# Kernel optimization log

Hardware: AMD Instinct MI355X
Metric: run time of the kernel (lower is better)

The kernel has to match this reference:

```python
import jax, jax.numpy as jnp
import numpy as np

DIM, HEADS, DH = 512, 8, 64  # head_dim = DIM // HEADS, power of 2
BATCH, SEQ = 2, 1024
RANK = 4  # TensorTrain rank
EPS = 1e-8


def setup_inputs() -> dict:
    key = jax.random.key(0)
    ks = jax.random.split(key, 13)
    inp = {"x": jax.random.normal(ks[0], (BATCH, SEQ, DIM), jnp.float32)}
    i = 1
    for n in ("q", "k", "v", "o"):
        inp[n + "A"] = jax.random.normal(ks[i], (DIM, RANK), jnp.float32) * 0.1
        inp[n + "B"] = jax.random.normal(ks[i + 1], (RANK, DIM), jnp.float32) * 0.1
        inp[n + "b"] = jax.random.normal(ks[i + 2], (DIM,), jnp.float32) * 0.02
        i += 3
    return inp


def _tt_linear(x, A, Bm, b):
    # QuantumInspiredLinear: W = A @ Bm (rank-4 TT reconstruction), y = x W^T + b
    w = A @ Bm  # [out, in]
    return jnp.einsum('bsd,od->bso', x, w) + b


def _embed(x):
    # quantum state preparation: L2-normalize amplitudes per state
    return x / (jnp.linalg.norm(x, axis=-1, keepdims=True) + EPS)


def _measure(x):
    # measurement: squared amplitudes normalized to a probability distribution
    sq = x * x
    return sq / (jnp.sum(sq, axis=-1, keepdims=True) + EPS)


def reference(x, qA, qB, qb, kA, kB, kb, vA, vB, vb, oA, oB, ob):
    bsz, seq, dim = x.shape
    q = _tt_linear(x, qA, qB, qb).reshape(-1, DH)  # [N, dh], N = B*S*H
    k = _tt_linear(x, kA, kB, kb).reshape(-1, DH)
    v = _tt_linear(x, vA, vB, vb).reshape(-1, DH)
    qq = _embed(q)
    kq = _embed(k)
    # flat global attention over N = batch*seq*heads rows (as written in source)
    attn = jax.nn.softmax(jnp.matmul(qq, kq.T) / np.float32(np.sqrt(DH)), axis=-1)
    attended = jnp.matmul(attn, v)           # [N, dh]
    attended = _measure(attended)
    out = attended.reshape(bsz, seq, dim)    # [B, S, D]
    return _tt_linear(out, oA, oB, ob)
```

## Files before the change

### kernel.cpp

```cpp
#include <hip/hip_runtime.h>
#include <math.h>

#define DIM    512
#define RANK   4
#define NROW   2048
#define DH     64
#define NH     16384
#define EPS    1e-8f
#define EPSDEN2 2.68435456f
#define KSCALE 0.0626220703125f
#define C1 (2.0f * KSCALE)
#define C2 (2.0f * KSCALE * KSCALE)
#define KSPL 32

typedef short    bf16x8 __attribute__((ext_vector_type(8)));
typedef ushort   u16x8  __attribute__((ext_vector_type(8)));
typedef _Float16 half8  __attribute__((ext_vector_type(8)));
typedef float    f32x16 __attribute__((ext_vector_type(16)));

static __device__ __forceinline__ ushort f2bf(float f) {
    uint u = __float_as_uint(f);
    u += 0x7FFFu + ((u >> 16) & 1u);
    return (ushort)(u >> 16);
}
static __device__ __forceinline__ float bf2f(ushort u) {
    return __uint_as_float((uint)u << 16);
}
static __device__ __forceinline__ uint pkh2(float a, float b) {
    _Float16 ha = (_Float16)a, hb = (_Float16)b;
    return (uint)__builtin_bit_cast(ushort, ha) | ((uint)__builtin_bit_cast(ushort, hb) << 16);
}
static __device__ __forceinline__ float h2f(ushort u) {
    return (float)__builtin_bit_cast(_Float16, u);
}
static __device__ __forceinline__ void barrier_lgkm() {
    asm volatile("s_waitcnt lgkmcnt(0)" ::: "memory");
    __builtin_amdgcn_s_barrier();
}

__global__ __launch_bounds__(256) void proj_qkv(
    const float* __restrict__ x,
    const float* __restrict__ qA, const float* __restrict__ qB, const float* __restrict__ qb,
    const float* __restrict__ kA, const float* __restrict__ kB, const float* __restrict__ kb,
    const float* __restrict__ vA, const float* __restrict__ vB, const float* __restrict__ vb,
    ushort* __restrict__ qq_b, ushort* __restrict__ kqT, ushort* __restrict__ vvT)
{
    __shared__ float qrow[DIM], krow[DIM], vrowS[DIM];
    __shared__ float wred[4][12];
    __shared__ float tvals[12];
    __shared__ float norms[16];

    const int n = blockIdx.x, t = threadIdx.x;
    const int wid = t >> 6, lane = t & 63;

    const float x0 = x[n * DIM + t];
    const float x1 = x[n * DIM + t + 256];

    float p[12];
    #pragma unroll
    for (int r = 0; r < 4; ++r) {
        p[r]     = x0 * qB[r * DIM + t] + x1 * qB[r * DIM + t + 256];
        p[4 + r] = x0 * kB[r * DIM + t] + x1 * kB[r * DIM + t + 256];
        p[8 + r] = x0 * vB[r * DIM + t] + x1 * vB[r * DIM + t + 256];
    }
    #pragma unroll
    for (int i = 0; i < 12; ++i) {
        #pragma unroll
        for (int off = 32; off; off >>= 1) p[i] += __shfl_xor(p[i], off);
    }
    if (lane == 0) {
        #pragma unroll
        for (int i = 0; i < 12; ++i) wred[wid][i] = p[i];
    }
    __syncthreads();
    if (t < 12) tvals[t] = wred[0][t] + wred[1][t] + wred[2][t] + wred[3][t];
    __syncthreads();

    float tq[4], tk[4], tv[4];
    #pragma unroll
    for (int r = 0; r < 4; ++r) { tq[r] = tvals[r]; tk[r] = tvals[4 + r]; tv[r] = tvals[8 + r]; }

    #pragma unroll
    for (int h = 0; h < 2; ++h) {
        const int o = t + h * 256;
        float yq = qb[o], yk = kb[o], yv = vb[o];
        #pragma unroll
        for (int r = 0; r < 4; ++r) {
            yq += tq[r] * qA[o * RANK + r];
            yk += tk[r] * kA[o * RANK + r];
            yv += tv[r] * vA[o * RANK + r];
        }
        qrow[o] = yq; krow[o] = yk; vrowS[o] = yv;
    }
    __syncthreads();

    {
        const int c = t >> 5, i2 = t & 31;
        const float a  = qrow[c * 64 + i2], b2 = qrow[c * 64 + i2 + 32];
        const float ak = krow[c * 64 + i2], bk = krow[c * 64 + i2 + 32];
        float s  = a * a + b2 * b2;
        float sk = ak * ak + bk * bk;
        #pragma unroll
        for (int off = 16; off; off >>= 1) { s += __shfl_xor(s, off); sk += __shfl_xor(sk, off); }
        if (i2 == 0) { norms[c] = sqrtf(s); norms[8 + c] = sqrtf(sk); }
    }
    __syncthreads();

    #pragma unroll
    for (int h = 0; h < 2; ++h) {
        const int o = t + h * 256;
        const int c = o >> 6;
        qq_b[n * DIM + o] = f2bf(qrow[o] / (norms[c] + EPS));
    }

    if (t < 64) {
        uint pk[4], pv[4];
        #pragma unroll
        for (int i = 0; i < 4; ++i) {
            const float k0 = krow[(2 * i) * 64 + t]     / (norms[8 + 2 * i] + EPS);
            const float k1 = krow[(2 * i + 1) * 64 + t] / (norms[8 + 2 * i + 1] + EPS);
            pk[i] = pkh2(k0, k1);
            pv[i] = pkh2(vrowS[(2 * i) * 64 + t], vrowS[(2 * i + 1) * 64 + t]);
        }
        uint4 uk; uk.x = pk[0]; uk.y = pk[1]; uk.z = pk[2]; uk.w = pk[3];
        uint4 uv; uv.x = pv[0]; uv.y = pv[1]; uv.z = pv[2]; uv.w = pv[3];
        *(uint4*)((char*)kqT + (size_t)t * (NH * 2) + (size_t)n * 16) = uk;
        *(uint4*)((char*)vvT + (size_t)t * (NH * 2) + (size_t)n * 16) = uv;
    }
}

__global__ __launch_bounds__(256, 2) void phaseA(
    const ushort* __restrict__ kqT, const ushort* __restrict__ vvT,
    ushort* __restrict__ partA, ushort* __restrict__ partM1)
{
    __shared__ __align__(16) char smem[2][10240];
    constexpr int NSTA = 16;

    const int t = threadIdx.x;
    const int w = t >> 6, l = t & 63;
    const int l31 = l & 31, hi = l >> 5;
    const int agroup = blockIdx.x >> 5;
    const int ksplit = blockIdx.x & 31;
    const int kbase = ksplit * 512;
    const bool isM1 = (agroup == 16);
    const int a = isM1 ? 0 : (agroup * 4 + w);
    const bool compute = (!isM1) || (w == 0);

    const int srow = t >> 2, sslot = t & 3;
    const int woff = srow * 80 + sslot * 16;
    const size_t go = (size_t)srow * NH + kbase + sslot * 8;

    f32x16 acc[2][2];
    #pragma unroll
    for (int bt = 0; bt < 2; ++bt)
        #pragma unroll
        for (int dt = 0; dt < 2; ++dt)
            #pragma unroll
            for (int r = 0; r < 16; ++r) acc[bt][dt][r] = 0.f;

    uint4 kst = *(const uint4*)(kqT + go);
    uint4 vst = *(const uint4*)(vvT + go);
    *(uint4*)(smem[0] + woff) = kst;
    *(uint4*)(smem[0] + 5120 + woff) = vst;
    kst = *(const uint4*)(kqT + go + 32);
    vst = *(const uint4*)(vvT + go + 32);
    barrier_lgkm();

    for (int s = 0; s < NSTA; ++s) {
        const char* B = smem[s & 1];
        if (s + 1 < NSTA) {
            char* D = (char*)smem[(s & 1) ^ 1];
            *(uint4*)(D + woff) = kst;
            *(uint4*)(D + 5120 + woff) = vst;
        }
        if (s + 2 < NSTA) {
            kst = *(const uint4*)(kqT + go + (size_t)(s + 2) * 32);
            vst = *(const uint4*)(vvT + go + (size_t)(s + 2) * 32);
        }
        if (compute) {
            half8 af[2][2], vf[2][2];
            if (!isM1) {
                const half8 bc0 = *(const half8*)(B + a * 80 + hi * 16);
                const half8 bc1 = *(const half8*)(B + a * 80 + 32 + hi * 16);
                #pragma unroll
                for (int bt = 0; bt < 2; ++bt) {
                    af[bt][0] = (*(const half8*)(B + (bt * 32 + l31) * 80 + hi * 16)) * bc0;
                    af[bt][1] = (*(const half8*)(B + (bt * 32 + l31) * 80 + 32 + hi * 16)) * bc1;
                }
            } else {
                #pragma unroll
                for (int bt = 0; bt < 2; ++bt) {
                    af[bt][0] = *(const half8*)(B + (bt * 32 + l31) * 80 + hi * 16);
                    af[bt][1] = *(const half8*)(B + (bt * 32 + l31) * 80 + 32 + hi * 16);
                }
            }
            #pragma unroll
            for (int dt = 0; dt < 2; ++dt) {
                vf[dt][0] = *(const half8*)(B + 5120 + (dt * 32 + l31) * 80 + hi * 16);
                vf[dt][1] = *(const half8*)(B + 5120 + (dt * 32 + l31) * 80 + 32 + hi * 16);
            }
            #pragma unroll
            for (int bt = 0; bt < 2; ++bt)
                #pragma unroll
                for (int dt = 0; dt < 2; ++dt) {
                    acc[bt][dt] = __builtin_amdgcn_mfma_f32_32x32x16_f16(af[bt][0], vf[dt][0], acc[bt][dt], 0, 0, 0);
                    acc[bt][dt] = __builtin_amdgcn_mfma_f32_32x32x16_f16(af[bt][1], vf[dt][1], acc[bt][dt], 0, 0, 0);
                }
        }
        barrier_lgkm();
    }

    if (compute) {
        ushort* dst = isM1 ? (partM1 + (size_t)ksplit * 4096)
                           : (partA + ((size_t)(ksplit * 64 + a)) * 4096);
        #pragma unroll
        for (int bt = 0; bt < 2; ++bt)
            #pragma unroll
            for (int dt = 0; dt < 2; ++dt) {
                const int d = dt * 32 + l31;
                #pragma unroll
                for (int g = 0; g < 4; ++g) {
                    uint2 u2;
                    u2.x = pkh2(acc[bt][dt][4 * g],     acc[bt][dt][4 * g + 1]);
                    u2.y = pkh2(acc[bt][dt][4 * g + 2], acc[bt][dt][4 * g + 3]);
                    const int b0 = bt * 32 + 8 * g + 4 * hi;
                    *(uint2*)(dst + (size_t)d * 64 + b0) = u2;
                }
            }
    }
}

__global__ __launch_bounds__(256) void reduce_mom(
    const ushort* __restrict__ partA, const ushort* __restrict__ partM1,
    ushort* __restrict__ T2s, ushort* __restrict__ M1s, float* __restrict__ Vpart)
{
    const int blk = blockIdx.x, t = threadIdx.x;
    if (blk < 256) {
        const int g = blk * 256 + t;
        const uint2* src = (const uint2*)partA;
        float s0 = 0.f, s1 = 0.f, s2 = 0.f, s3 = 0.f;
        #pragma unroll
        for (int ks = 0; ks < KSPL; ++ks) {
            const uint2 u = src[(size_t)ks * 65536 + g];
            s0 += h2f((ushort)(u.x & 0xffff));
            s1 += h2f((ushort)(u.x >> 16));
            s2 += h2f((ushort)(u.y & 0xffff));
            s3 += h2f((ushort)(u.y >> 16));
        }
        uint2 o;
        o.x = (uint)f2bf(C2 * s0) | ((uint)f2bf(C2 * s1) << 16);
        o.y = (uint)f2bf(C2 * s2) | ((uint)f2bf(C2 * s3) << 16);
        ((uint2*)T2s)[g] = o;
        const int a  = g >> 10;
        const int d  = (g >> 4) & 63;
        const int b0 = (g & 15) * 4;
        if (a >= b0 && a < b0 + 4) {
            const int r = a - b0;
            const float sd = (r == 0) ? s0 : (r == 1) ? s1 : (r == 2) ? s2 : s3;
            Vpart[a * 64 + d] = sd;
        }
    } else {
        const int g = (blk - 256) * 256 + t;
        const uint2* src = (const uint2*)partM1;
        float s0 = 0.f, s1 = 0.f, s2 = 0.f, s3 = 0.f;
        #pragma unroll
        for (int ks = 0; ks < KSPL; ++ks) {
            const uint2 u = src[(size_t)ks * 1024 + g];
            s0 += h2f((ushort)(u.x & 0xffff));
            s1 += h2f((ushort)(u.x >> 16));
            s2 += h2f((ushort)(u.y & 0xffff));
            s3 += h2f((ushort)(u.y >> 16));
        }
        uint2 o;
        o.x = (uint)f2bf(C1 * s0) | ((uint)f2bf(C1 * s1) << 16);
        o.y = (uint)f2bf(C1 * s2) | ((uint)f2bf(C1 * s3) << 16);
        ((uint2*)M1s)[g] = o;
    }
}

__global__ __launch_bounds__(256, 3) void phaseB(
    const ushort* __restrict__ qq_b, const ushort* __restrict__ T2s,
    const ushort* __restrict__ M1s, const float* __restrict__ Vpart,
    const float* __restrict__ oA, const float* __restrict__ oB,
    const float* __restrict__ ob, float* __restrict__ out)
{
    __shared__ float Lred[4][64][33];
    __shared__ float anum[32][65];
    __shared__ float VsumL[64];

    const int t = threadIdx.x;
    const int w = t >> 6, l = t & 63;
    const int l31 = l & 31, hi = l >> 5;
    const int q0 = blockIdx.x * 32;
    const int n0 = q0 >> 3;

    if (w == 3) {
        float vs = 0.f;
        #pragma unroll
        for (int a2 = 0; a2 < 64; ++a2) vs += Vpart[a2 * 64 + l];
        VsumL[l] = vs;
    }

    bf16x8 Qf[4];
    #pragma unroll
    for (int w16 = 0; w16 < 4; ++w16)
        Qf[w16] = *(const bf16x8*)((const char*)qq_b
            + (size_t)(q0 + l31) * 128 + w16 * 32 + hi * 16);

    float sv[16];
    {
        const uint4 u0 = *(const uint4*)(qq_b + (size_t)(q0 + l31) * 64 + w * 16);
        const uint4 u1 = *(const uint4*)(qq_b + (size_t)(q0 + l31) * 64 + w * 16 + 8);
        sv[0] = bf2f((ushort)(u0.x & 0xffff)); sv[1] = bf2f((ushort)(u0.x >> 16));
        sv[2] = bf2f((ushort)(u0.y & 0xffff)); sv[3] = bf2f((ushort)(u0.y >> 16));
        sv[4] = bf2f((ushort)(u0.z & 0xffff)); sv[5] = bf2f((ushort)(u0.z >> 16));
        sv[6] = bf2f((ushort)(u0.w & 0xffff)); sv[7] = bf2f((ushort)(u0.w >> 16));
        sv[8]  = bf2f((ushort)(u1.x & 0xffff)); sv[9]  = bf2f((ushort)(u1.x >> 16));
        sv[10] = bf2f((ushort)(u1.y & 0xffff)); sv[11] = bf2f((ushort)(u1.y >> 16));
        sv[12] = bf2f((ushort)(u1.z & 0xffff)); sv[13] = bf2f((ushort)(u1.z >> 16));
        sv[14] = bf2f((ushort)(u1.w & 0xffff)); sv[15] = bf2f((ushort)(u1.w >> 16));
    }

    f32x16 acc[2];
    #pragma unroll
    for (int dt = 0; dt < 2; ++dt)
        #pragma unroll
        for (int r = 0; r < 16; ++r) acc[dt][r] = 0.f;

    #pragma unroll 2
    for (int ai = 0; ai < 16; ++ai) {
        const char* base = (const char*)(T2s + (size_t)(w * 16 + ai) * 4096);
        #pragma unroll
        for (int dt = 0; dt < 2; ++dt) {
            bf16x8 af[4];
            #pragma unroll
            for (int w16 = 0; w16 < 4; ++w16)
                af[w16] = *(const bf16x8*)(base + (dt * 32 + l31) * 128 + w16 * 32 + hi * 16);
            f32x16 st;
            #pragma unroll
            for (int r = 0; r < 16; ++r) st[r] = 0.f;
            #pragma unroll
            for (int w16 = 0; w16 < 4; ++w16)
                st = __builtin_amdgcn_mfma_f32_32x32x16_bf16(af[w16], Qf[w16], st, 0, 0, 0);
            #pragma unroll
            for (int r = 0; r < 16; ++r)
                acc[dt][r] = fmaf(sv[ai], st[r], acc[dt][r]);
        }
    }

    if (w == 0) {
        #pragma unroll
        for (int dt = 0; dt < 2; ++dt) {
            bf16x8 af[4];
            #pragma unroll
            for (int w16 = 0; w16 < 4; ++w16)
                af[w16] = *(const bf16x8*)((const char*)M1s + (dt * 32 + l31) * 128 + w16 * 32 + hi * 16);
            f32x16 st;
            #pragma unroll
            for (int r = 0; r < 16; ++r) st[r] = 0.f;
            #pragma unroll
            for (int w16 = 0; w16 < 4; ++w16)
                st = __builtin_amdgcn_mfma_f32_32x32x16_bf16(af[w16], Qf[w16], st, 0, 0, 0);
            #pragma unroll
            for (int r = 0; r < 16; ++r) acc[dt][r] += st[r];
        }
    }

    #pragma unroll
    for (int dt = 0; dt < 2; ++dt)
        #pragma unroll
        for (int r = 0; r < 16; ++r) {
            const int d = dt * 32 + 8 * (r >> 2) + 4 * hi + (r & 3);
            Lred[w][d][l31] = acc[dt][r];
        }
    __syncthreads();

    {
        const int q = t >> 3, db = (t & 7) * 8;
        float av[8];
        float ss = 0.f;
        #pragma unroll
        for (int i = 0; i < 8; ++i) {
            const int d = db + i;
            const float s = (Lred[0][d][q] + Lred[1][d][q])
                          + (Lred[2][d][q] + Lred[3][d][q]) + VsumL[d];
            av[i] = s;
            ss = fmaf(s, s, ss);
        }
        ss += __shfl_xor(ss, 1);
        ss += __shfl_xor(ss, 2);
        ss += __shfl_xor(ss, 4);
        const float inv = 1.f / (ss + EPSDEN2);
        #pragma unroll
        for (int i = 0; i < 8; ++i) anum[q][db + i] = av[i] * av[i] * inv;
    }
    __syncthreads();

    {
        float p0 = 0.f, p1 = 0.f, p2 = 0.f, p3 = 0.f;
        #pragma unroll
        for (int h2 = 0; h2 < 8; ++h2) {
            const int o = h2 * 64 + l;
            const float m = anum[w * 8 + h2][l];
            p0 = fmaf(m, oB[o],        p0);
            p1 = fmaf(m, oB[512 + o],  p1);
            p2 = fmaf(m, oB[1024 + o], p2);
            p3 = fmaf(m, oB[1536 + o], p3);
        }
        #pragma unroll
        for (int off = 32; off; off >>= 1) {
            p0 += __shfl_xor(p0, off);
            p1 += __shfl_xor(p1, off);
            p2 += __shfl_xor(p2, off);
            p3 += __shfl_xor(p3, off);
        }
        float* dstrow = out + (size_t)(n0 + w) * DIM;
        #pragma unroll
        for (int h2 = 0; h2 < 8; ++h2) {
            const int o = h2 * 64 + l;
            const float4 a4 = *(const float4*)(oA + o * RANK);
            dstrow[o] = ob[o] + p0 * a4.x + p1 * a4.y + p2 * a4.z + p3 * a4.w;
        }
    }
}

extern "C" void kernel_launch(void* const* d_in, const int* in_sizes, int n_in,
                              void* d_out, int out_size, void* d_ws, size_t ws_size,
                              hipStream_t stream) {
    const float* x  = (const float*)d_in[0];
    const float* qA = (const float*)d_in[1];
    const float* qB = (const float*)d_in[2];
    const float* qb = (const float*)d_in[3];
    const float* kA = (const float*)d_in[4];
    const float* kB = (const float*)d_in[5];
    const float* kb = (const float*)d_in[6];
    const float* vA = (const float*)d_in[7];
    const float* vB = (const float*)d_in[8];
    const float* vb = (const float*)d_in[9];
    const float* oA = (const float*)d_in[10];
    const float* oB = (const float*)d_in[11];
    const float* ob = (const float*)d_in[12];

    ushort* qq_b   = (ushort*)d_ws;
    ushort* kqT    = qq_b + (size_t)NH * DH;
    ushort* vvT    = kqT + (size_t)NH * DH;
    ushort* T2s    = vvT + (size_t)NH * DH;
    ushort* M1s    = T2s + (size_t)64 * 4096;
    ushort* partM1 = M1s + 4096;
    float*  Vpart  = (float*)(partM1 + (size_t)KSPL * 4096);
    ushort* partA  = (ushort*)(Vpart + 4096);

    float* out = (float*)d_out;

    proj_qkv<<<NROW, 256, 0, stream>>>(x, qA, qB, qb, kA, kB, kb, vA, vB, vb, qq_b, kqT, vvT);
    phaseA<<<17 * KSPL, 256, 0, stream>>>(kqT, vvT, partA, partM1);
    reduce_mom<<<260, 256, 0, stream>>>(partA, partM1, T2s, M1s, Vpart);
    phaseB<<<512, 256, 0, stream>>>(qq_b, T2s, M1s, Vpart, oA, oB, ob, out);
}
```

Before: 79.22 us.

## Fuse moment reduction into phaseA via atomic counter and fold M1 into wave 0

```diff
diff --git a/kernel.cpp b/kernel.cpp
--- a/kernel.cpp
+++ b/kernel.cpp
@@ -12,6 +12,8 @@
 #define C1 (2.0f * KSCALE)
 #define C2 (2.0f * KSCALE * KSCALE)
 #define KSPL 32
+#define NBLK_A 512
+#define NRED 64
 
 typedef short    bf16x8 __attribute__((ext_vector_type(8)));
 typedef ushort   u16x8  __attribute__((ext_vector_type(8)));
@@ -131,9 +133,12 @@
 
 __global__ __launch_bounds__(256, 2) void phaseA(
     const ushort* __restrict__ kqT, const ushort* __restrict__ vvT,
-    ushort* __restrict__ partA, ushort* __restrict__ partM1)
+    ushort* __restrict__ partA, ushort* __restrict__ partM1,
+    ushort* __restrict__ T2s, ushort* __restrict__ M1s,
+    float* __restrict__ Vpart, uint* __restrict__ ctr)
 {
     __shared__ __align__(16) char smem[2][10240];
+    __shared__ uint sOld;
     constexpr int NSTA = 16;
 
     const int t = threadIdx.x;
@@ -142,21 +147,20 @@
     const int agroup = blockIdx.x >> 5;
     const int ksplit = blockIdx.x & 31;
     const int kbase = ksplit * 512;
-    const bool isM1 = (agroup == 16);
-    const int a = isM1 ? 0 : (agroup * 4 + w);
-    const bool compute = (!isM1) || (w == 0);
+    const int a = agroup * 4 + w;
+    const bool doM1 = (agroup == 0) && (w == 0);
 
     const int srow = t >> 2, sslot = t & 3;
     const int woff = srow * 80 + sslot * 16;
     const size_t go = (size_t)srow * NH + kbase + sslot * 8;
 
-    f32x16 acc[2][2];
+    f32x16 acc[2][2], accM[2][2];
     #pragma unroll
     for (int bt = 0; bt < 2; ++bt)
         #pragma unroll
         for (int dt = 0; dt < 2; ++dt)
             #pragma unroll
-            for (int r = 0; r < 16; ++r) acc[bt][dt][r] = 0.f;
+            for (int r = 0; r < 16; ++r) { acc[bt][dt][r] = 0.f; accM[bt][dt][r] = 0.f; }
 
     uint4 kst = *(const uint4*)(kqT + go);
     uint4 vst = *(const uint4*)(vvT + go);
@@ -177,42 +181,43 @@
             kst = *(const uint4*)(kqT + go + (size_t)(s + 2) * 32);
             vst = *(const uint4*)(vvT + go + (size_t)(s + 2) * 32);
         }
-        if (compute) {
-            half8 af[2][2], vf[2][2];
-            if (!isM1) {
-                const half8 bc0 = *(const half8*)(B + a * 80 + hi * 16);
-                const half8 bc1 = *(const half8*)(B + a * 80 + 32 + hi * 16);
-                #pragma unroll
-                for (int bt = 0; bt < 2; ++bt) {
-                    af[bt][0] = (*(const half8*)(B + (bt * 32 + l31) * 80 + hi * 16)) * bc0;
-                    af[bt][1] = (*(const half8*)(B + (bt * 32 + l31) * 80 + 32 + hi * 16)) * bc1;
-                }
-            } else {
-                #pragma unroll
-                for (int bt = 0; bt < 2; ++bt) {
-                    af[bt][0] = *(const half8*)(B + (bt * 32 + l31) * 80 + hi * 16);
-                    af[bt][1] = *(const half8*)(B + (bt * 32 + l31) * 80 + 32 + hi * 16);
-                }
+
+        half8 kraw[2][2], af[2][2], vf[2][2];
+        const half8 bc0 = *(const half8*)(B + a * 80 + hi * 16);
+        const half8 bc1 = *(const half8*)(B + a * 80 + 32 + hi * 16);
+        #pragma unroll
+        for (int bt = 0; bt < 2; ++bt) {
+            kraw[bt][0] = *(const half8*)(B + (bt * 32 + l31) * 80 + hi * 16);
+            kraw[bt][1] = *(const half8*)(B + (bt * 32 + l31) * 80 + 32 + hi * 16);
+            af[bt][0] = kraw[bt][0] * bc0;
+            af[bt][1] = kraw[bt][1] * bc1;
+        }
+        #pragma unroll
+        for (int dt = 0; dt < 2; ++dt) {
+            vf[dt][0] = *(const half8*)(B + 5120 + (dt * 32 + l31) * 80 + hi * 16);
+            vf[dt][1] = *(const half8*)(B + 5120 + (dt * 32 + l31) * 80 + 32 + hi * 16);
+        }
+        #pragma unroll
+        for (int bt = 0; bt < 2; ++bt)
+            #pragma unroll
+            for (int dt = 0; dt < 2; ++dt) {
+                acc[bt][dt] = __builtin_amdgcn_mfma_f32_32x32x16_f16(af[bt][0], vf[dt][0], acc[bt][dt], 0, 0, 0);
+                acc[bt][dt] = __builtin_amdgcn_mfma_f32_32x32x16_f16(af[bt][1], vf[dt][1], acc[bt][dt], 0, 0, 0);
             }
-            #pragma unroll
-            for (int dt = 0; dt < 2; ++dt) {
-                vf[dt][0] = *(const half8*)(B + 5120 + (dt * 32 + l31) * 80 + hi * 16);
-                vf[dt][1] = *(const half8*)(B + 5120 + (dt * 32 + l31) * 80 + 32 + hi * 16);
-            }
+        if (doM1) {
             #pragma unroll
             for (int bt = 0; bt < 2; ++bt)
                 #pragma unroll
                 for (int dt = 0; dt < 2; ++dt) {
-                    acc[bt][dt] = __builtin_amdgcn_mfma_f32_32x32x16_f16(af[bt][0], vf[dt][0], acc[bt][dt], 0, 0, 0);
-                    acc[bt][dt] = __builtin_amdgcn_mfma_f32_32x32x16_f16(af[bt][1], vf[dt][1], acc[bt][dt], 0, 0, 0);
+                    accM[bt][dt] = __builtin_amdgcn_mfma_f32_32x32x16_f16(kraw[bt][0], vf[dt][0], accM[bt][dt], 0, 0, 0);
+                    accM[bt][dt] = __builtin_amdgcn_mfma_f32_32x32x16_f16(kraw[bt][1], vf[dt][1], accM[bt][dt], 0, 0, 0);
                 }
         }
         barrier_lgkm();
     }
 
-    if (compute) {
-        ushort* dst = isM1 ? (partM1 + (size_t)ksplit * 4096)
-                           : (partA + ((size_t)(ksplit * 64 + a)) * 4096);
+    {
+        ushort* dst = partA + ((size_t)(ksplit * 64 + a)) * 4096;
         #pragma unroll
         for (int bt = 0; bt < 2; ++bt)
             #pragma unroll
@@ -228,15 +233,42 @@
                 }
             }
     }
-}
-
-__global__ __launch_bounds__(256) void reduce_mom(
-    const ushort* __restrict__ partA, const ushort* __restrict__ partM1,
-    ushort* __restrict__ T2s, ushort* __restrict__ M1s, float* __restrict__ Vpart)
-{
-    const int blk = blockIdx.x, t = threadIdx.x;
-    if (blk < 256) {
-        const int g = blk * 256 + t;
+    if (doM1) {
+        ushort* dstM = partM1 + (size_t)ksplit * 4096;
+        #pragma unroll
+        for (int bt = 0; bt < 2; ++bt)
+            #pragma unroll
+            for (int dt = 0; dt < 2; ++dt) {
+                const int d = dt * 32 + l31;
+                #pragma unroll
+                for (int g = 0; g < 4; ++g) {
+                    uint2 u2;
+                    u2.x = pkh2(accM[bt][dt][4 * g],     accM[bt][dt][4 * g + 1]);
+                    u2.y = pkh2(accM[bt][dt][4 * g + 2], accM[bt][dt][4 * g + 3]);
+                    const int b0 = bt * 32 + 8 * g + 4 * hi;
+                    *(uint2*)(dstM + (size_t)d * 64 + b0) = u2;
+                }
+            }
+    }
+
+    __threadfence();
+    if (t == 0)
+        sOld = __hip_atomic_fetch_add(ctr, 1u, __ATOMIC_ACQ_REL, __HIP_MEMORY_SCOPE_AGENT);
+    __syncthreads();
+    const uint old = sOld;
+    if (old < (uint)(NBLK_A - NRED)) return;
+    const uint rank = old - (uint)(NBLK_A - NRED);
+
+    if (t == 0) {
+        while (__hip_atomic_load(ctr, __ATOMIC_ACQUIRE, __HIP_MEMORY_SCOPE_AGENT) < (uint)NBLK_A)
+            __builtin_amdgcn_s_sleep(16);
+    }
+    __syncthreads();
+    __threadfence();
+
+    #pragma unroll
+    for (int k2 = 0; k2 < 4; ++k2) {
+        const int g = (int)rank * 1024 + k2 * 256 + t;
         const uint2* src = (const uint2*)partA;
         float s0 = 0.f, s1 = 0.f, s2 = 0.f, s3 = 0.f;
         #pragma unroll
@@ -251,16 +283,17 @@
         o.x = (uint)f2bf(C2 * s0) | ((uint)f2bf(C2 * s1) << 16);
         o.y = (uint)f2bf(C2 * s2) | ((uint)f2bf(C2 * s3) << 16);
         ((uint2*)T2s)[g] = o;
-        const int a  = g >> 10;
+        const int a2 = g >> 10;
         const int d  = (g >> 4) & 63;
         const int b0 = (g & 15) * 4;
-        if (a >= b0 && a < b0 + 4) {
-            const int r = a - b0;
+        if (a2 >= b0 && a2 < b0 + 4) {
+            const int r = a2 - b0;
             const float sd = (r == 0) ? s0 : (r == 1) ? s1 : (r == 2) ? s2 : s3;
-            Vpart[a * 64 + d] = sd;
-        }
-    } else {
-        const int g = (blk - 256) * 256 + t;
+            Vpart[a2 * 64 + d] = sd;
+        }
+    }
+    if (rank < 4) {
+        const int g = (int)rank * 256 + t;
         const uint2* src = (const uint2*)partM1;
         float s0 = 0.f, s1 = 0.f, s2 = 0.f, s3 = 0.f;
         #pragma unroll
@@ -448,12 +481,13 @@
     ushort* M1s    = T2s + (size_t)64 * 4096;
     ushort* partM1 = M1s + 4096;
     float*  Vpart  = (float*)(partM1 + (size_t)KSPL * 4096);
-    ushort* partA  = (ushort*)(Vpart + 4096);
+    uint*   ctr    = (uint*)(Vpart + 4096);
+    ushort* partA  = (ushort*)(ctr + 64);
 
     float* out = (float*)d_out;
 
+    hipMemsetAsync(ctr, 0, sizeof(uint), stream);
     proj_qkv<<<NROW, 256, 0, stream>>>(x, qA, qB, qb, kA, kB, kb, vA, vB, vb, qq_b, kqT, vvT);
-    phaseA<<<17 * KSPL, 256, 0, stream>>>(kqT, vvT, partA, partM1);
-    reduce_mom<<<260, 256, 0, stream>>>(partA, partM1, T2s, M1s, Vpart);
+    phaseA<<<NBLK_A, 256, 0, stream>>>(kqT, vvT, partA, partM1, T2s, M1s, Vpart, ctr);
     phaseB<<<512, 256, 0, stream>>>(qq_b, T2s, M1s, Vpart, oA, oB, ob, out);
 }
```

New measurement: 188.0 us. 137% more time.
